# Optimization experiments

Measured on AMD Instinct MI355X. Metric: run time of the kernel, lower is better.

## Reference

```python
import jax, jax.numpy as jnp
import numpy as np

NUM_USERS = 8000
NUM_ITEMS = 4000
EMB_DIM = 64
NUM_LAYERS = 3
NUM_EDGES = 300000
N = NUM_USERS + NUM_ITEMS


def setup_inputs() -> dict:
    key = jax.random.key(0)
    k1, k2, k3 = jax.random.split(key, 3)
    edge_index = jax.random.randint(k1, (2, NUM_EDGES), 0, N, dtype=jnp.int64 if jax.config.jax_enable_x64 else jnp.int32)
    # xavier-uniform-like init
    bound = float(np.sqrt(6.0 / (NUM_USERS + EMB_DIM)))
    user_emb = jax.random.uniform(k2, (NUM_USERS, EMB_DIM), jnp.float32, -bound, bound)
    bound_i = float(np.sqrt(6.0 / (NUM_ITEMS + EMB_DIM)))
    item_emb = jax.random.uniform(k3, (NUM_ITEMS, EMB_DIM), jnp.float32, -bound_i, bound_i)
    return {"edge_index": edge_index, "user_emb": user_emb, "item_emb": item_emb}


def _normalized_adj(edge_index):
    # dense symmetric adjacency from edge list, then D^{-1/2} A D^{-1/2}
    adj = jnp.zeros((N, N), jnp.float32)
    adj = adj.at[edge_index[0], edge_index[1]].set(1.0)
    adj = adj.at[edge_index[1], edge_index[0]].set(1.0)
    degree = jnp.clip(adj.sum(axis=1, keepdims=True), 1.0)  # (N,1)
    dsqrt = jnp.sqrt(degree)
    return adj / dsqrt / dsqrt.T


def reference(edge_index, user_emb, item_emb):
    adj = _normalized_adj(edge_index)
    all_emb = jnp.concatenate([user_emb, item_emb], axis=0)  # (N, d)
    acc = all_emb
    cur = all_emb
    for _ in range(NUM_LAYERS):
        cur = adj @ cur
        acc = acc + cur
    final = acc / (NUM_LAYERS + 1)  # mean over layer outputs
    return final[:NUM_USERS], final[NUM_USERS:]
```

## Files before the change

### kernel.cpp

```cpp
#include <hip/hip_runtime.h>
#include <hip/hip_bf16.h>

namespace {

constexpr int NU = 8000;
constexpr int NI = 4000;
constexpr int NN = 12000;
constexpr int D  = 64;
constexpr int NE = 300000;
constexpr int STRIDE = 128;

__device__ __forceinline__ int probe_e32(const unsigned* raw, int lane) {
    unsigned v = raw[2 * lane + 1];
    return (__ballot(v != 0u) != 0ull) ? 1 : 0;
}
__device__ __forceinline__ int probe_f32(const unsigned short* ue, int lane) {
    int e = (ue[2 * lane] >> 7) & 0xFF;
    return (__ballot(e > 126) != 0ull) ? 1 : 0;
}

__global__ __launch_bounds__(256) void scatter_init(const unsigned* __restrict__ raw,
                                                    const unsigned short* __restrict__ ue,
                                                    const unsigned short* __restrict__ ie,
                                                    unsigned* __restrict__ fill,
                                                    int* __restrict__ col,
                                                    unsigned short* __restrict__ x0,
                                                    float* __restrict__ out) {
    const int tid  = blockIdx.x * blockDim.x + threadIdx.x;
    const int NT   = gridDim.x * blockDim.x;
    const int lane = threadIdx.x & 63;
    const int e32  = probe_e32(raw, lane);
    const int f32  = probe_f32(ue, lane);
    const unsigned base = fill[NN];

    for (int t = tid; t < NE; t += NT) {
        int a, b;
        if (e32) { a = (int)raw[t];     b = (int)raw[NE + t]; }
        else     { a = (int)raw[2 * t]; b = (int)raw[2 * NE + 2 * t]; }
        unsigned s = atomicAdd(&fill[a], 1u) - base;
        if (s < STRIDE) col[a * STRIDE + s] = b;
        if (a != b) {
            s = atomicAdd(&fill[b], 1u) - base;
            if (s < STRIDE) col[b * STRIDE + s] = a;
        }
    }
    for (int q = tid; q < NN * D / 4; q += NT) {
        int i = q * 4;
        float4 vf;
        ushort4 vb;
        if (f32) {
            const float* src = (i < NU * D) ? ((const float*)ue) + i
                                            : ((const float*)ie) + (i - NU * D);
            vf = *(const float4*)src;
            vb.x = __bfloat16_as_ushort(__float2bfloat16(vf.x));
            vb.y = __bfloat16_as_ushort(__float2bfloat16(vf.y));
            vb.z = __bfloat16_as_ushort(__float2bfloat16(vf.z));
            vb.w = __bfloat16_as_ushort(__float2bfloat16(vf.w));
        } else {
            const unsigned short* src = (i < NU * D) ? ue + i : ie + (i - NU * D);
            vb = *(const ushort4*)src;
            vf.x = __uint_as_float(((unsigned)vb.x) << 16);
            vf.y = __uint_as_float(((unsigned)vb.y) << 16);
            vf.z = __uint_as_float(((unsigned)vb.z) << 16);
            vf.w = __uint_as_float(((unsigned)vb.w) << 16);
        }
        *(ushort4*)(x0 + i) = vb;
        *(float4*)(out + i) = vf;
    }
}

__global__ __launch_bounds__(256) void dedup(const unsigned* __restrict__ fill,
                                             int* __restrict__ col,
                                             float* __restrict__ dinv,
                                             unsigned short* __restrict__ x0) {
    __shared__ unsigned bits[4][376];
    __shared__ int cnt[4];
    const int lane = threadIdx.x & 63;
    const int wave = __builtin_amdgcn_readfirstlane(threadIdx.x >> 6);
    const int row  = blockIdx.x * 4 + wave;
    unsigned* bb = bits[wave];
    for (int w = lane; w < 376; w += 64) bb[w] = 0;
    if (lane == 0) cnt[wave] = 0;
    const unsigned base = fill[NN];
    unsigned nn = fill[row] - base;
    int n = (int)(nn < (unsigned)STRIDE ? nn : (unsigned)STRIDE);
    const int cbase = row * STRIDE;
    for (int cb = 0; cb < n; cb += 64) {
        int idx = cb + lane;
        if (idx < n) {
            int c = col[cbase + idx];
            unsigned bit = 1u << (c & 31);
            unsigned old = atomicOr(&bb[c >> 5], bit);
            if (!(old & bit)) {
                int pos = atomicAdd(&cnt[wave], 1);
                col[cbase + pos] = c;
            }
        }
    }
    int d = cnt[wave];
    float dr = rsqrtf((float)(d > 0 ? d : 1));
    if (lane == 0) dinv[row] = dr;
    const int o = row * D + lane;
    float v = __uint_as_float(((unsigned)x0[o]) << 16);
    x0[o] = __bfloat16_as_ushort(__float2bfloat16(dr * v));
}

__global__ __launch_bounds__(256) void spmm(const unsigned* __restrict__ degu_unused,
                                            const float* __restrict__ dinv,
                                            const int* __restrict__ col,
                                            const unsigned short* __restrict__ zin,
                                            unsigned short* __restrict__ zout,
                                            float* __restrict__ out,
                                            const unsigned* __restrict__ fill,
                                            int final_layer) {
    const int lane = threadIdx.x & 63;
    const int wave = __builtin_amdgcn_readfirstlane(threadIdx.x >> 6);
    const int row  = blockIdx.x * 4 + wave;
    const float dr = dinv[row];
    const float drf = 1.0f / (dr * dr);
    const int n = (int)(drf + 0.5f);
    const int base = row * STRIDE;
    float sum = 0.f;
    #pragma unroll 4
    for (int j = 0; j < n; ++j) {
        int   c = col[base + j];
        float v = __uint_as_float(((unsigned)zin[c * D + lane]) << 16);
        sum += v;
    }
    const int o = row * D + lane;
    float y = dr * sum;
    if (final_layer) {
        out[o] = (out[o] + y) * 0.25f;
    } else {
        zout[o] = (unsigned short)__bfloat16_as_ushort(__float2bfloat16(dr * y));
        out[o] += y;
    }
}

}

extern "C" void kernel_launch(void* const* d_in, const int* in_sizes, int n_in,
                              void* d_out, int out_size, void* d_ws, size_t ws_size,
                              hipStream_t stream) {
    int ei = 0, ui = 1, ii = 2;
    for (int i = 0; i < n_in; ++i) {
        if      (in_sizes[i] == 2 * NE) ei = i;
        else if (in_sizes[i] == NU * D) ui = i;
        else if (in_sizes[i] == NI * D) ii = i;
    }
    const unsigned*       raw = (const unsigned*)d_in[ei];
    const unsigned short* ue  = (const unsigned short*)d_in[ui];
    const unsigned short* ie  = (const unsigned short*)d_in[ii];
    float*                out = (float*)d_out;

    char* ws = (char*)d_ws;
    size_t off = 0;
    auto take = [&](size_t bytes) {
        void* p = ws + off;
        off += (bytes + 15) & ~(size_t)15;
        return p;
    };
    unsigned*       fill = (unsigned*)take((NN + 1) * 4);
    float*          dinv = (float*)take(NN * 4);
    int*            col  = (int*)take((size_t)NN * STRIDE * 4);
    unsigned short* x0   = (unsigned short*)take((size_t)NN * D * 2);
    unsigned short* x1   = (unsigned short*)take((size_t)NN * D * 2);
    (void)ws_size;

    scatter_init<<<1024, 256, 0, stream>>>(raw, ue, ie, fill, col, x0, out);
    dedup<<<NN / 4, 256, 0, stream>>>(fill, col, dinv, x0);

    spmm<<<NN / 4, 256, 0, stream>>>(nullptr, dinv, col, x0, x1, out, fill, 0);
    spmm<<<NN / 4, 256, 0, stream>>>(nullptr, dinv, col, x1, x0, out, fill, 0);
    spmm<<<NN / 4, 256, 0, stream>>>(nullptr, dinv, col, x0, nullptr, out, fill, 1);
}
```

Measured before the change: 140.3 us.

## Process four neighbors per wave with 8-byte loads and zero-row padding

The SpMM kernel now splits each 64-lane wave into four 16-lane groups. Each group gathers a different neighbor row with an 8-byte load covering four bf16 features, and the partial sums are combined with cross-lane shuffles. Neighbor lists are padded to a multiple of four with a sentinel index that points at an extra all-zero row added to both feature buffers. The goal is more memory-level parallelism and fewer loop iterations per row, in exchange for shuffle reductions, partially idle lanes in the epilogue, and up to three wasted padded loads per row.

```diff
diff --git a/kernel.cpp b/kernel.cpp
--- a/kernel.cpp
+++ b/kernel.cpp
@@ -25,6 +25,7 @@
                                                     unsigned* __restrict__ fill,
                                                     int* __restrict__ col,
                                                     unsigned short* __restrict__ x0,
+                                                    unsigned short* __restrict__ x1,
                                                     float* __restrict__ out) {
     const int tid  = blockIdx.x * blockDim.x + threadIdx.x;
     const int NT   = gridDim.x * blockDim.x;
@@ -66,6 +67,10 @@
         }
         *(ushort4*)(x0 + i) = vb;
         *(float4*)(out + i) = vf;
+    }
+    if (tid < D / 4) {
+        *(ushort4*)(x0 + NN * D + 4 * tid) = make_ushort4(0, 0, 0, 0);
+        *(ushort4*)(x1 + NN * D + 4 * tid) = make_ushort4(0, 0, 0, 0);
     }
 }
 
@@ -98,6 +103,8 @@
         }
     }
     int d = cnt[wave];
+    int n4 = (d + 3) & ~3;
+    if (lane < n4 - d) col[cbase + d + lane] = NN;
     float dr = rsqrtf((float)(d > 0 ? d : 1));
     if (lane == 0) dinv[row] = dr;
     const int o = row * D + lane;
@@ -105,35 +112,60 @@
     x0[o] = __bfloat16_as_ushort(__float2bfloat16(dr * v));
 }
 
-__global__ __launch_bounds__(256) void spmm(const unsigned* __restrict__ degu_unused,
-                                            const float* __restrict__ dinv,
+__global__ __launch_bounds__(256) void spmm(const float* __restrict__ dinv,
                                             const int* __restrict__ col,
                                             const unsigned short* __restrict__ zin,
                                             unsigned short* __restrict__ zout,
                                             float* __restrict__ out,
-                                            const unsigned* __restrict__ fill,
                                             int final_layer) {
     const int lane = threadIdx.x & 63;
     const int wave = __builtin_amdgcn_readfirstlane(threadIdx.x >> 6);
     const int row  = blockIdx.x * 4 + wave;
+    const int quarter = lane >> 4;
+    const int sub     = lane & 15;
     const float dr = dinv[row];
-    const float drf = 1.0f / (dr * dr);
-    const int n = (int)(drf + 0.5f);
+    const int d  = (int)(1.0f / (dr * dr) + 0.5f);
+    const int n4 = (d + 3) & ~3;
     const int base = row * STRIDE;
-    float sum = 0.f;
+    float s0 = 0.f, s1 = 0.f, s2 = 0.f, s3 = 0.f;
     #pragma unroll 4
-    for (int j = 0; j < n; ++j) {
-        int   c = col[base + j];
-        float v = __uint_as_float(((unsigned)zin[c * D + lane]) << 16);
-        sum += v;
-    }
-    const int o = row * D + lane;
-    float y = dr * sum;
-    if (final_layer) {
-        out[o] = (out[o] + y) * 0.25f;
-    } else {
-        zout[o] = (unsigned short)__bfloat16_as_ushort(__float2bfloat16(dr * y));
-        out[o] += y;
+    for (int j = 0; j < n4; j += 4) {
+        int c = col[base + j + quarter];
+        uint2 u = *(const uint2*)(zin + c * D + 4 * sub);
+        s0 += __uint_as_float(u.x << 16);
+        s1 += __uint_as_float(u.x & 0xFFFF0000u);
+        s2 += __uint_as_float(u.y << 16);
+        s3 += __uint_as_float(u.y & 0xFFFF0000u);
+    }
+    s0 += __shfl(s0, lane ^ 16, 64);  s1 += __shfl(s1, lane ^ 16, 64);
+    s2 += __shfl(s2, lane ^ 16, 64);  s3 += __shfl(s3, lane ^ 16, 64);
+    s0 += __shfl(s0, lane ^ 32, 64);  s1 += __shfl(s1, lane ^ 32, 64);
+    s2 += __shfl(s2, lane ^ 32, 64);  s3 += __shfl(s3, lane ^ 32, 64);
+    if (lane < 16) {
+        const int o = row * D + 4 * sub;
+        float4 prev = *(const float4*)(out + o);
+        float y0 = dr * s0, y1 = dr * s1, y2 = dr * s2, y3 = dr * s3;
+        if (final_layer) {
+            float4 r;
+            r.x = (prev.x + y0) * 0.25f;
+            r.y = (prev.y + y1) * 0.25f;
+            r.z = (prev.z + y2) * 0.25f;
+            r.w = (prev.w + y3) * 0.25f;
+            *(float4*)(out + o) = r;
+        } else {
+            ushort4 zb;
+            zb.x = __bfloat16_as_ushort(__float2bfloat16(dr * y0));
+            zb.y = __bfloat16_as_ushort(__float2bfloat16(dr * y1));
+            zb.z = __bfloat16_as_ushort(__float2bfloat16(dr * y2));
+            zb.w = __bfloat16_as_ushort(__float2bfloat16(dr * y3));
+            *(ushort4*)(zout + o) = zb;
+            float4 r;
+            r.x = prev.x + y0;
+            r.y = prev.y + y1;
+            r.z = prev.z + y2;
+            r.w = prev.w + y3;
+            *(float4*)(out + o) = r;
+        }
     }
 }
 
@@ -163,14 +195,14 @@
     unsigned*       fill = (unsigned*)take((NN + 1) * 4);
     float*          dinv = (float*)take(NN * 4);
     int*            col  = (int*)take((size_t)NN * STRIDE * 4);
-    unsigned short* x0   = (unsigned short*)take((size_t)NN * D * 2);
-    unsigned short* x1   = (unsigned short*)take((size_t)NN * D * 2);
+    unsigned short* x0   = (unsigned short*)take((size_t)(NN + 1) * D * 2);
+    unsigned short* x1   = (unsigned short*)take((size_t)(NN + 1) * D * 2);
     (void)ws_size;
 
-    scatter_init<<<1024, 256, 0, stream>>>(raw, ue, ie, fill, col, x0, out);
+    scatter_init<<<1024, 256, 0, stream>>>(raw, ue, ie, fill, col, x0, x1, out);
     dedup<<<NN / 4, 256, 0, stream>>>(fill, col, dinv, x0);
 
-    spmm<<<NN / 4, 256, 0, stream>>>(nullptr, dinv, col, x0, x1, out, fill, 0);
-    spmm<<<NN / 4, 256, 0, stream>>>(nullptr, dinv, col, x1, x0, out, fill, 0);
-    spmm<<<NN / 4, 256, 0, stream>>>(nullptr, dinv, col, x0, nullptr, out, fill, 1);
-}
+    spmm<<<NN / 4, 256, 0, stream>>>(dinv, col, x0, x1, out, 0);
+    spmm<<<NN / 4, 256, 0, stream>>>(dinv, col, x1, x0, out, 0);
+    spmm<<<NN / 4, 256, 0, stream>>>(dinv, col, x0, nullptr, out, 1);
+}
```

Measured after the change: 134.6 us. 1.04x faster.
